# Kernel optimization log

Measured on AMD Instinct MI355X. Metric: run time of the kernel, lower is better.

The kernel has to match this reference:

```python
import jax, jax.numpy as jnp
import numpy as np
from jax import lax

DT = 0.1  # forward() default dt


def setup_inputs() -> dict:
    key = jax.random.key(0)
    k1, k2, k3 = jax.random.split(key, 3)
    B, S = 256, 65536
    strain = jax.random.normal(k1, (B, S), dtype=jnp.float32)
    strain_rate = jax.random.normal(k2, (B, S), dtype=jnp.float32)
    log_E = jnp.zeros((1,), dtype=jnp.float32)            # E = 1.0
    log_eta = jnp.log(jnp.full((1,), 10.0, jnp.float32))  # eta = 10.0
    return {"strain": strain, "strain_rate": strain_rate,
            "log_E": log_E, "log_eta": log_eta}


def reference(strain, strain_rate, log_E, log_eta):
    # Maxwell element: stress[0] = E*strain[0] + eta*rate[0]
    #                  stress[t] = a*stress[t-1] + E*(strain[t]-strain[t-1]),  a = exp(-dt/tau)
    E = jnp.exp(log_E)          # (1,)
    eta = jnp.exp(log_eta)      # (1,)
    tau = eta / E
    a = jnp.exp(-DT / tau)      # (1,) constant decay

    B, S = strain.shape
    # driving term u[t]
    u0 = E * strain[:, :1] + eta * strain_rate[:, :1]          # (B,1)
    u_rest = E * (strain[:, 1:] - strain[:, :-1])              # (B,S-1)
    u = jnp.concatenate([u0, u_rest], axis=1)                  # (B,S)
    # decay coeffs: first step has no history
    A = jnp.concatenate([jnp.ones((B, 1), strain.dtype),
                         jnp.broadcast_to(a, (B, S - 1))], axis=1)

    def combine(x, y):
        a1, b1 = x
        a2, b2 = y
        return a1 * a2, b2 + a2 * b1

    _, stress = lax.associative_scan(combine, (A, u), axis=1)  # (B,S)
    return stress
```

## Files before the change

### kernel.cpp

```cpp
#include <hip/hip_runtime.h>
#include <math.h>


#define DT_F  0.1f
#define S_LEN 65536
#define B_ROWS 256
#define CHUNK 1024
#define WARM  512
#define CPR   (S_LEN / CHUNK)

typedef float nfloat4 __attribute__((ext_vector_type(4)));

template<int CTRL, int RM>
__device__ __forceinline__ float dpp0(float x) {
    return __int_as_float(__builtin_amdgcn_update_dpp(
        0, __float_as_int(x), CTRL, RM, 0xF, false));
}
template<int N>
__device__ __forceinline__ float dpp_shr(float x) { return dpp0<0x110 + N, 0xF>(x); }
__device__ __forceinline__ float bcast15(float x) { return dpp0<0x142, 0xA>(x); }
__device__ __forceinline__ float bcast31(float x) { return dpp0<0x143, 0xC>(x); }
__device__ __forceinline__ float wshr1(float x)   { return dpp0<0x138, 0xF>(x); }
__device__ __forceinline__ float rdl(float x, int l) {
    return __int_as_float(__builtin_amdgcn_readlane(__float_as_int(x), l));
}

__global__ __launch_bounds__(256) void maxwell_scan(
    const float* __restrict__ strain,
    const float* __restrict__ rate,
    const float* __restrict__ log_E,
    const float* __restrict__ log_eta,
    float* __restrict__ out)
{
    const int lane = threadIdx.x & 63;
    const int wid  = blockIdx.x * 4 + (threadIdx.x >> 6);
    const int row  = wid / CPR;
    const int c    = wid % CPR;

    const float E   = __expf(log_E[0]);
    const float eta = __expf(log_eta[0]);
    const float lam = -DT_F * E / eta;
    const float a   = __expf(lam);
    const float a2 = a * a, a3 = a2 * a, a4 = a2 * a2, a8 = a4 * a4;
    const float a16 = a8 * a8, a32 = a16 * a16, a64 = a32 * a32;
    const float a128 = a64 * a64, a256 = a128 * a128;
    const float cc = E * (a - 1.0f);
    const float cca1 = cc * a, cca2 = cc * a2, cca3 = cc * a3;

    const int  lrow = lane & 15;
    const float alane = __expf(lam * (float)(4 * lane));
    const float wX    = __expf(lam * (float)(4 * lrow));
    const float wm1   = wX * a4;
    const float wm2   = (lane >= 48) ? wm1 * a64 : wm1;

    const int rowbase = row * S_LEN;
    const int t0 = c * CHUNK;
    const nfloat4* s4 = (const nfloat4*)(strain + rowbase);
    nfloat4*       o4 = (nfloat4*)(out + rowbase);

    nfloat4 w0, w1;
    if (c != 0) {
        const int vw = ((t0 - WARM) >> 2) + lane;
        w0 = s4[vw]; w1 = s4[vw + 64];
    }
    const int vp = (t0 >> 2) + lane;
    nfloat4 p0 = s4[vp +   0], p1 = s4[vp +  64], p2 = s4[vp + 128], p3 = s4[vp + 192];

    float S = 0.0f;

    auto scanW = [&](float fl3) -> float {
        float D = fl3, v;
        v = dpp_shr<1>(D); D = fmaf(a4,  v, D);
        v = dpp_shr<2>(D); D = fmaf(a8,  v, D);
        v = dpp_shr<4>(D); D = fmaf(a16, v, D);
        v = dpp_shr<8>(D); D = fmaf(a32, v, D);
        v = bcast15(D);    D = fmaf(wm1, v, D);
        v = bcast31(D);    D = fmaf(wm2, v, D);
        return D;
    };

    if (c != 0) {
        auto warmg = [&](nfloat4 wf) {
            float fl = wf.x;
            fl = fmaf(a, fl, wf.y); fl = fmaf(a, fl, wf.z); fl = fmaf(a, fl, wf.w);
            float W = scanW(fl);
            float T = rdl(W, 63);
            S = fmaf(a256, S, T);
        };
        warmg(w0); warmg(w1);
    }

    float etar0 = 0.0f;
    if (c == 0) etar0 = eta * rate[rowbase];
    const float rl0 = etar0 * alane;
    const float rl1 = rl0 * a, rl2 = rl0 * a2, rl3 = rl0 * a3;
    float base = 1.0f;

    auto payg = [&](nfloat4 pf, int vo) {
        float fl0 = pf.x;
        float fl1 = fmaf(a, fl0, pf.y);
        float fl2 = fmaf(a, fl1, pf.z);
        float fl3 = fmaf(a, fl2, pf.w);
        float W = scanW(fl3);
        float T = rdl(W, 63);
        float X = wshr1(W);
        float Xs = fmaf(alane, S, X);
        nfloat4 o;
        o.x = fmaf(cc,   Xs, E * pf.x);
        o.y = fmaf(cca1, Xs, fmaf(cc, fl0, E * pf.y));
        o.z = fmaf(cca2, Xs, fmaf(cc, fl1, E * pf.z));
        o.w = fmaf(cca3, Xs, fmaf(cc, fl2, E * pf.w));
        o.x = fmaf(base, rl0, o.x);
        o.y = fmaf(base, rl1, o.y);
        o.z = fmaf(base, rl2, o.z);
        o.w = fmaf(base, rl3, o.w);
        o4[vo] = o;
        S = fmaf(a256, S, T);
        base *= a256;
    };
    payg(p0, vp +   0); payg(p1, vp +  64); payg(p2, vp + 128); payg(p3, vp + 192);
}

extern "C" void kernel_launch(void* const* d_in, const int* in_sizes, int n_in,
                              void* d_out, int out_size, void* d_ws, size_t ws_size,
                              hipStream_t stream) {
    const float* strain  = (const float*)d_in[0];
    const float* rate    = (const float*)d_in[1];
    const float* log_E   = (const float*)d_in[2];
    const float* log_eta = (const float*)d_in[3];
    float* out = (float*)d_out;

    const int total_chunks = B_ROWS * CPR;
    const int blocks = total_chunks / 4;
    maxwell_scan<<<blocks, 256, 0, stream>>>(strain, rate, log_E, log_eta, out);
}
```

Before: 156.8 us.

## Share chunk carries across waves in a block via LDS instead of per-wave warmup

The four waves in a block now handle consecutive chunks of the same row. Only wave 0 runs the 512-element warm-up to estimate the incoming state. The other waves take their carry from the per-group totals of earlier waves, exchanged through LDS after a barrier. This removes three quarters of the redundant warm-up loads and scans. In exchange it adds a __syncthreads and a short serial prefix loop over earlier waves, and the waves in a block become dependent on each other.

```diff
diff --git a/kernel.cpp b/kernel.cpp
--- a/kernel.cpp
+++ b/kernel.cpp
@@ -7,7 +7,9 @@
 #define B_ROWS 256
 #define CHUNK 1024
 #define WARM  512
+#define WPB   4
 #define CPR   (S_LEN / CHUNK)
+#define BPR   (CPR / WPB)
 
 typedef float nfloat4 __attribute__((ext_vector_type(4)));
 
@@ -32,10 +34,14 @@
     const float* __restrict__ log_eta,
     float* __restrict__ out)
 {
+    __shared__ float Tlds[WPB * 4];
+    __shared__ float S0lds;
+
     const int lane = threadIdx.x & 63;
-    const int wid  = blockIdx.x * 4 + (threadIdx.x >> 6);
-    const int row  = wid / CPR;
-    const int c    = wid % CPR;
+    const int wv   = threadIdx.x >> 6;
+    const int row  = blockIdx.x / BPR;
+    const int cb   = (blockIdx.x % BPR) * WPB;
+    const int c    = cb + wv;
 
     const float E   = __expf(log_E[0]);
     const float eta = __expf(log_eta[0]);
@@ -44,6 +50,7 @@
     const float a2 = a * a, a3 = a2 * a, a4 = a2 * a2, a8 = a4 * a4;
     const float a16 = a8 * a8, a32 = a16 * a16, a64 = a32 * a32;
     const float a128 = a64 * a64, a256 = a128 * a128;
+    const float a512 = a256 * a256, a768 = a512 * a256, a1024 = a512 * a512;
     const float cc = E * (a - 1.0f);
     const float cca1 = cc * a, cca2 = cc * a2, cca3 = cc * a3;
 
@@ -59,14 +66,16 @@
     nfloat4*       o4 = (nfloat4*)(out + rowbase);
 
     nfloat4 w0, w1;
-    if (c != 0) {
+    const bool do_warm = (wv == 0) && (cb != 0);
+    if (do_warm) {
         const int vw = ((t0 - WARM) >> 2) + lane;
         w0 = s4[vw]; w1 = s4[vw + 64];
     }
     const int vp = (t0 >> 2) + lane;
     nfloat4 p0 = s4[vp +   0], p1 = s4[vp +  64], p2 = s4[vp + 128], p3 = s4[vp + 192];
 
-    float S = 0.0f;
+    float etar0 = 0.0f;
+    if (c == 0) etar0 = eta * rate[rowbase];
 
     auto scanW = [&](float fl3) -> float {
         float D = fl3, v;
@@ -78,47 +87,64 @@
         v = bcast31(D);    D = fmaf(wm2, v, D);
         return D;
     };
+    auto groupW = [&](nfloat4 pf) -> float {
+        float fl = pf.x;
+        fl = fmaf(a, fl, pf.y); fl = fmaf(a, fl, pf.z); fl = fmaf(a, fl, pf.w);
+        return scanW(fl);
+    };
 
-    if (c != 0) {
-        auto warmg = [&](nfloat4 wf) {
-            float fl = wf.x;
-            fl = fmaf(a, fl, wf.y); fl = fmaf(a, fl, wf.z); fl = fmaf(a, fl, wf.w);
-            float W = scanW(fl);
-            float T = rdl(W, 63);
-            S = fmaf(a256, S, T);
-        };
-        warmg(w0); warmg(w1);
+    float W0 = groupW(p0), W1 = groupW(p1), W2 = groupW(p2), W3 = groupW(p3);
+    if (lane == 63) {
+        Tlds[wv * 4 + 0] = W0; Tlds[wv * 4 + 1] = W1;
+        Tlds[wv * 4 + 2] = W2; Tlds[wv * 4 + 3] = W3;
     }
+    float S0 = 0.0f;
+    if (do_warm) {
+        float Tw0 = rdl(groupW(w0), 63);
+        float Tw1 = rdl(groupW(w1), 63);
+        S0 = fmaf(a256, Tw0, Tw1);
+    }
+    if (threadIdx.x == 0) S0lds = S0;
+    __syncthreads();
 
-    float etar0 = 0.0f;
-    if (c == 0) etar0 = eta * rate[rowbase];
+    float S = S0lds;
+    for (int j = 0; j < wv; ++j) {
+        float Tc = Tlds[j * 4 + 0];
+        Tc = fmaf(a256, Tc, Tlds[j * 4 + 1]);
+        Tc = fmaf(a256, Tc, Tlds[j * 4 + 2]);
+        Tc = fmaf(a256, Tc, Tlds[j * 4 + 3]);
+        S = fmaf(a1024, S, Tc);
+    }
+    const float T0 = Tlds[wv * 4 + 0], T1 = Tlds[wv * 4 + 1], T2 = Tlds[wv * 4 + 2];
+    const float Sg0 = S;
+    const float Sg1 = fmaf(a256, Sg0, T0);
+    const float Sg2 = fmaf(a256, Sg1, T1);
+    const float Sg3 = fmaf(a256, Sg2, T2);
+
     const float rl0 = etar0 * alane;
     const float rl1 = rl0 * a, rl2 = rl0 * a2, rl3 = rl0 * a3;
-    float base = 1.0f;
 
-    auto payg = [&](nfloat4 pf, int vo) {
+    auto outg = [&](nfloat4 pf, float W, float Sg, float bse, int vo) {
         float fl0 = pf.x;
         float fl1 = fmaf(a, fl0, pf.y);
         float fl2 = fmaf(a, fl1, pf.z);
-        float fl3 = fmaf(a, fl2, pf.w);
-        float W = scanW(fl3);
-        float T = rdl(W, 63);
-        float X = wshr1(W);
-        float Xs = fmaf(alane, S, X);
+        float X  = wshr1(W);
+        float Xs = fmaf(alane, Sg, X);
         nfloat4 o;
         o.x = fmaf(cc,   Xs, E * pf.x);
         o.y = fmaf(cca1, Xs, fmaf(cc, fl0, E * pf.y));
         o.z = fmaf(cca2, Xs, fmaf(cc, fl1, E * pf.z));
         o.w = fmaf(cca3, Xs, fmaf(cc, fl2, E * pf.w));
-        o.x = fmaf(base, rl0, o.x);
-        o.y = fmaf(base, rl1, o.y);
-        o.z = fmaf(base, rl2, o.z);
-        o.w = fmaf(base, rl3, o.w);
+        o.x = fmaf(bse, rl0, o.x);
+        o.y = fmaf(bse, rl1, o.y);
+        o.z = fmaf(bse, rl2, o.z);
+        o.w = fmaf(bse, rl3, o.w);
         o4[vo] = o;
-        S = fmaf(a256, S, T);
-        base *= a256;
     };
-    payg(p0, vp +   0); payg(p1, vp +  64); payg(p2, vp + 128); payg(p3, vp + 192);
+    outg(p0, W0, Sg0, 1.0f, vp +   0);
+    outg(p1, W1, Sg1, a256, vp +  64);
+    outg(p2, W2, Sg2, a512, vp + 128);
+    outg(p3, W3, Sg3, a768, vp + 192);
 }
 
 extern "C" void kernel_launch(void* const* d_in, const int* in_sizes, int n_in,
@@ -130,7 +156,6 @@
     const float* log_eta = (const float*)d_in[3];
     float* out = (float*)d_out;
 
-    const int total_chunks = B_ROWS * CPR;
-    const int blocks = total_chunks / 4;
+    const int blocks = B_ROWS * BPR;
     maxwell_scan<<<blocks, 256, 0, stream>>>(strain, rate, log_E, log_eta, out);
 }
```

New measurement: 156.2 us. No clear change (-0.4%).
